# Performance work log

Measured on AMD Instinct MI355X. Metric: run time of the kernel, lower is better.

## Reference

```python
import jax, jax.numpy as jnp
import numpy as np

WS = 7  # window size
NH = 4  # num heads


def _relative_position_index(ws: int) -> np.ndarray:
    coords = np.stack(np.meshgrid(np.arange(ws), np.arange(ws), indexing='ij'))  # [2,ws,ws]
    coords = coords.reshape(2, -1)
    rel = coords[:, :, None] - coords[:, None, :]  # [2,N,N]
    rel = rel.transpose(1, 2, 0) + (ws - 1)
    rel[:, :, 0] *= 2 * ws - 1
    return rel.sum(-1)  # [N,N] in [0,(2ws-1)^2)


REL_IDX = _relative_position_index(WS)


def setup_inputs() -> dict:
    key = jax.random.key(0)
    k1, k2, k3, k4 = jax.random.split(key, 4)
    dim = 128
    x = jax.random.normal(k1, (64, 56, 56, dim), dtype=jnp.float32)
    qkv_w = jax.random.normal(k2, (dim, 3 * dim), dtype=jnp.float32) * (dim ** -0.5)
    qkv_b = jnp.zeros((3 * dim,), dtype=jnp.float32)
    proj_w = jax.random.normal(k3, (dim, dim), dtype=jnp.float32) * (dim ** -0.5)
    proj_b = jnp.zeros((dim,), dtype=jnp.float32)
    bias_table = jax.random.truncated_normal(k4, -2.0, 2.0, ((2 * WS - 1) ** 2, NH), dtype=jnp.float32) * 0.02
    return {"x": x, "qkv_w": qkv_w, "qkv_b": qkv_b, "proj_w": proj_w, "proj_b": proj_b, "bias_table": bias_table}


def reference(x, qkv_w, qkv_b, proj_w, proj_b, bias_table):
    B, H, W, C = x.shape
    ws, nh = WS, NH
    hd = C // nh
    N = ws * ws
    # window partition: [B*nWh*nWw, N, C]  (H,W divisible by ws -> no padding branch)
    xw = x.reshape(B, H // ws, ws, W // ws, ws, C).transpose(0, 1, 3, 2, 4, 5).reshape(-1, N, C)
    qkv = xw @ qkv_w + qkv_b  # [nW, N, 3C]
    qkv = qkv.reshape(-1, N, 3, nh, hd).transpose(2, 0, 3, 1, 4)  # [3, nW, nh, N, hd]
    q, k, v = qkv[0], qkv[1], qkv[2]
    attn = jnp.einsum('whqd,whkd->whqk', q, k) * (hd ** -0.5)  # [nW, nh, N, N]
    rel_bias = bias_table[REL_IDX.reshape(-1)].reshape(N, N, nh).transpose(2, 0, 1)  # [nh,N,N]
    attn = jax.nn.softmax(attn + rel_bias[None], axis=-1)
    out = jnp.einsum('whqk,whkd->whqd', attn, v)  # [nW, nh, N, hd]
    out = out.transpose(0, 2, 1, 3).reshape(-1, N, C)
    out = out @ proj_w + proj_b
    # window reverse
    out = out.reshape(B, H // ws, W // ws, ws, ws, C).transpose(0, 1, 3, 2, 4, 5).reshape(B, H, W, C)
    return out
```

## Files before the change

kernel.cpp:

```cpp
#include <hip/hip_runtime.h>
#include <hip/hip_bf16.h>

#define NTOK 49
#define NPAD 64
#define CDIM 128
#define C3   384
#define NHEAD 4
#define HDIM 32
#define SCALE 0.17677669529663687f

#define QS 136
#define VS 72
#define PS 72

typedef __attribute__((ext_vector_type(8))) __bf16 bf16x8;
typedef __attribute__((ext_vector_type(4))) __bf16 bf16x4;
typedef __attribute__((ext_vector_type(4))) float f32x4;

#define PIN(v) asm volatile("" : "+v"(v))


__global__ __launch_bounds__(256) void prep_kernel(
    const float* __restrict__ qkv_w, const float* __restrict__ proj_w,
    const float* __restrict__ bias_table,
    __bf16* __restrict__ qkvT, __bf16* __restrict__ projT, float* __restrict__ blut)
{
  int o = blockIdx.x * 256 + threadIdx.x;
  if (o < CDIM * C3) {
    int n = o >> 7, k = o & 127;
    float v = qkv_w[k * C3 + n];
    if (n < CDIM) v *= SCALE;
    qkvT[o] = (__bf16)v;
  } else if (o < CDIM * C3 + CDIM * CDIM) {
    int o2 = o - CDIM * C3;
    int n = o2 >> 7, k = o2 & 127;
    projT[o2] = (__bf16)proj_w[k * CDIM + n];
  } else if (o < CDIM * C3 + CDIM * CDIM + NHEAD * NPAD * NPAD) {
    int t3 = o - (CDIM * C3 + CDIM * CDIM);
    int h = t3 >> 12, r = (t3 >> 6) & 63, c = t3 & 63;
    float v;
    if (c >= NTOK) v = -1e30f;
    else if (r >= NTOK) v = 0.0f;
    else {
      int idx = (r / 7 - c / 7 + 6) * 13 + (r % 7 - c % 7 + 6);
      v = bias_table[idx * NHEAD + h];
    }
    blut[t3] = v;
  }
}

__global__ __launch_bounds__(512, 4) void attn_kernel(
    const float* __restrict__ x, const float* __restrict__ qkv_b,
    const float* __restrict__ proj_b,
    const __bf16* __restrict__ qkvT, const __bf16* __restrict__ projT,
    const float* __restrict__ blut, float* __restrict__ out)
{
  __shared__ __align__(16) char smem[71680];
  __bf16* qs_ = (__bf16*)smem;
  __bf16* ks_ = qs_ + NPAD * QS;
  __bf16* vT_ = ks_ + NPAD * QS;
  char*   un_ = (char*)(vT_ + CDIM * VS);
  __bf16* xa_ = (__bf16*)un_;
  __bf16* Pm_ = (__bf16*)un_;

  const int tid  = threadIdx.x;
  const int wave = tid >> 6;
  const int lane = tid & 63;
  const int l15  = lane & 15;
  const int lg   = lane >> 4;

  const int win = blockIdx.x;
  const int b  = win >> 6;
  const int wh = (win >> 3) & 7;
  const int ww = win & 7;
  const float* xbase = x + (((b * 56) + wh * 7) * 56 + ww * 7) * CDIM;

  #pragma unroll
  for (int p = 0; p < 2; ++p) {
    int L = p * 512 + tid;
    int r = L >> 4, c = L & 15;
    bf16x8 v8;
    if (r < NTOK) {
      const float* g = xbase + ((r / 7) * 56 + (r % 7)) * CDIM + c * 8;
      f32x4 x0 = *(const f32x4*)g;
      f32x4 x1 = *(const f32x4*)(g + 4);
      v8[0] = (__bf16)x0[0]; v8[1] = (__bf16)x0[1]; v8[2] = (__bf16)x0[2]; v8[3] = (__bf16)x0[3];
      v8[4] = (__bf16)x1[0]; v8[5] = (__bf16)x1[1]; v8[6] = (__bf16)x1[2]; v8[7] = (__bf16)x1[3];
    } else {
      #pragma unroll
      for (int q2 = 0; q2 < 8; ++q2) v8[q2] = (__bf16)0.0f;
    }
    *(bf16x8*)(xa_ + r * QS + c * 8) = v8;
  }

  const int nb = wave * 48;
  bf16x8 bq[3][4];
  #pragma unroll
  for (int nt = 0; nt < 3; ++nt)
    #pragma unroll
    for (int kt = 0; kt < 4; ++kt) {
      bq[nt][kt] = *(const bf16x8*)(qkvT + (nb + nt * 16 + l15) * CDIM + kt * 32 + lg * 8);
      PIN(bq[nt][kt]);
    }
  float qb[3];
  #pragma unroll
  for (int nt = 0; nt < 3; ++nt) {
    qb[nt] = qkv_b[nb + nt * 16 + l15];
    if (nb + nt * 16 < CDIM) qb[nt] *= SCALE;
  }

  __syncthreads();

  #pragma unroll 2
  for (int mt = 0; mt < 4; ++mt) {
    bf16x8 a[4];
    #pragma unroll
    for (int kt = 0; kt < 4; ++kt)
      a[kt] = *(const bf16x8*)(xa_ + (mt * 16 + l15) * QS + kt * 32 + lg * 8);

    f32x4 acc[3];
    #pragma unroll
    for (int nt = 0; nt < 3; ++nt) { acc[nt][0]=0.f; acc[nt][1]=0.f; acc[nt][2]=0.f; acc[nt][3]=0.f; }
    #pragma unroll
    for (int nt = 0; nt < 3; ++nt)
      #pragma unroll
      for (int kt = 0; kt < 4; ++kt)
        acc[nt] = __builtin_amdgcn_mfma_f32_16x16x32_bf16(a[kt], bq[nt][kt], acc[nt], 0, 0, 0);

    const int r0 = mt * 16 + lg * 4;
    #pragma unroll
    for (int nt = 0; nt < 3; ++nt) {
      const int n = nb + nt * 16 + l15;
      if (n < CDIM) {
        #pragma unroll
        for (int i = 0; i < 4; ++i)
          qs_[(r0 + i) * QS + n] = (__bf16)(acc[nt][i] + qb[nt]);
      } else if (n < 2 * CDIM) {
        #pragma unroll
        for (int i = 0; i < 4; ++i)
          ks_[(r0 + i) * QS + (n - CDIM)] = (__bf16)(acc[nt][i] + qb[nt]);
      } else {
        bf16x4 vv;
        #pragma unroll
        for (int i = 0; i < 4; ++i) vv[i] = (__bf16)(acc[nt][i] + qb[nt]);
        *(bf16x4*)(vT_ + (n - 2 * CDIM) * VS + r0) = vv;
      }
    }
  }
  __syncthreads();

  const int nb2 = wave * 16;
  bf16x8 bp[4];
  #pragma unroll
  for (int kt = 0; kt < 4; ++kt) {
    bp[kt] = *(const bf16x8*)(projT + (nb2 + l15) * CDIM + kt * 32 + lg * 8);
    PIN(bp[kt]);
  }
  const float pb = proj_b[nb2 + l15];

  __bf16* O_ = qs_;

  {
    const int h  = wave & 3;
    const int hc = h * HDIM;
    const float* blh = blut + h * 4096;
    __bf16* Pw = Pm_ + wave * 16 * PS;

    bf16x8 bk[4];
    #pragma unroll
    for (int nt = 0; nt < 4; ++nt)
      bk[nt] = *(const bf16x8*)(ks_ + (nt * 16 + l15) * QS + hc + lg * 8);
    bf16x8 bv[2][2];
    #pragma unroll
    for (int n16 = 0; n16 < 2; ++n16)
      #pragma unroll
      for (int kt = 0; kt < 2; ++kt)
        bv[n16][kt] = *(const bf16x8*)(vT_ + (hc + n16 * 16 + l15) * VS + kt * 32 + lg * 8);

    #pragma unroll
    for (int mi = 0; mi < 2; ++mi) {
      const int mt = (wave >> 2) * 2 + mi;
      const int m0 = mt * 16;

      float bias[4][4];
      #pragma unroll
      for (int i = 0; i < 4; ++i) {
        const int r = m0 + lg * 4 + i;
        #pragma unroll
        for (int c = 0; c < 4; ++c) bias[i][c] = blh[r * 64 + c * 16 + l15];
      }

      bf16x8 aqf = *(const bf16x8*)(qs_ + (m0 + l15) * QS + hc + lg * 8);
      f32x4 s[4];
      #pragma unroll
      for (int nt = 0; nt < 4; ++nt) {
        f32x4 z; z[0]=0.f; z[1]=0.f; z[2]=0.f; z[3]=0.f;
        s[nt] = __builtin_amdgcn_mfma_f32_16x16x32_bf16(aqf, bk[nt], z, 0, 0, 0);
      }
      float inv[4];
      #pragma unroll
      for (int i = 0; i < 4; ++i) {
        const int lr = lg * 4 + i;
        float e0 = __expf(s[0][i] + bias[i][0]);
        float e1 = __expf(s[1][i] + bias[i][1]);
        float e2 = __expf(s[2][i] + bias[i][2]);
        float e3 = __expf(s[3][i] + bias[i][3]);
        Pw[lr * PS +      l15] = (__bf16)e0;
        Pw[lr * PS + 16 + l15] = (__bf16)e1;
        Pw[lr * PS + 32 + l15] = (__bf16)e2;
        Pw[lr * PS + 48 + l15] = (__bf16)e3;
        float sum = (e0 + e1) + (e2 + e3);
        #pragma unroll
        for (int off = 1; off < 16; off <<= 1) sum += __shfl_xor(sum, off);
        inv[i] = __builtin_amdgcn_rcpf(sum);
      }
      f32x4 o0, o1;
      o0[0]=0.f;o0[1]=0.f;o0[2]=0.f;o0[3]=0.f; o1[0]=0.f;o1[1]=0.f;o1[2]=0.f;o1[3]=0.f;
      #pragma unroll
      for (int kt = 0; kt < 2; ++kt) {
        bf16x8 ap = *(const bf16x8*)(Pw + l15 * PS + kt * 32 + lg * 8);
        o0 = __builtin_amdgcn_mfma_f32_16x16x32_bf16(ap, bv[0][kt], o0, 0, 0, 0);
        o1 = __builtin_amdgcn_mfma_f32_16x16x32_bf16(ap, bv[1][kt], o1, 0, 0, 0);
      }
      const int r0 = m0 + lg * 4;
      #pragma unroll
      for (int i = 0; i < 4; ++i) {
        O_[(r0 + i) * QS + hc +      l15] = (__bf16)(o0[i] * inv[i]);
        O_[(r0 + i) * QS + hc + 16 + l15] = (__bf16)(o1[i] * inv[i]);
      }
    }
  }
  __syncthreads();

  float* outw = out + (((b * 56) + wh * 7) * 56 + ww * 7) * CDIM;
  #pragma unroll
  for (int mt = 0; mt < 4; ++mt) {
    bf16x8 ao[4];
    #pragma unroll
    for (int kt = 0; kt < 4; ++kt)
      ao[kt] = *(const bf16x8*)(O_ + (mt * 16 + l15) * QS + kt * 32 + lg * 8);
    f32x4 c0;
    c0[0]=0.f;c0[1]=0.f;c0[2]=0.f;c0[3]=0.f;
    #pragma unroll
    for (int kt = 0; kt < 4; ++kt)
      c0 = __builtin_amdgcn_mfma_f32_16x16x32_bf16(ao[kt], bp[kt], c0, 0, 0, 0);
    #pragma unroll
    for (int i = 0; i < 4; ++i) {
      const int r = mt * 16 + lg * 4 + i;
      if (r < NTOK) {
        float* po = outw + ((r / 7) * 56 + (r % 7)) * CDIM + nb2;
        po[l15] = c0[i] + pb;
      }
    }
  }
}

extern "C" void kernel_launch(void* const* d_in, const int* in_sizes, int n_in,
                              void* d_out, int out_size, void* d_ws, size_t ws_size,
                              hipStream_t stream) {
  const float* x          = (const float*)d_in[0];
  const float* qkv_w      = (const float*)d_in[1];
  const float* qkv_b      = (const float*)d_in[2];
  const float* proj_w     = (const float*)d_in[3];
  const float* proj_b     = (const float*)d_in[4];
  const float* bias_table = (const float*)d_in[5];

  __bf16* qkvT  = (__bf16*)d_ws;
  __bf16* projT = qkvT + C3 * CDIM;
  float*  blut  = (float*)((char*)d_ws + 131072);
  float*  out   = (float*)d_out;

  hipLaunchKernelGGL(prep_kernel, dim3(320), dim3(256), 0, stream,
                     qkv_w, proj_w, bias_table, qkvT, projT, blut);
  hipLaunchKernelGGL(attn_kernel, dim3(4096), dim3(512), 0, stream,
                     x, qkv_b, proj_b, qkvT, projT, blut, out);
}
```

Before: 267.0 us.

## Reorder QKV projection to alias shared buffers and raise occupancy

Splits the QKV projection so K and V are computed and stored first, while Q stays in registers until the x tile is no longer needed. This lets x share memory with Q and P share memory with V, cutting LDS per block so the launch bound can target 6 blocks per CU instead of 4. The score MFMA is transposed (K as the A operand), which makes the bias loads vectorised and the softmax row sums a two-step cross-lane reduction instead of a four-step one. It also makes the prep kernel's weight reads coalesced and its writes strided. In exchange it adds an extra barrier, keeps Q accumulators live across it (more register pressure), and the tighter launch bound risks spills.

```diff
diff --git a/kernel.cpp b/kernel.cpp
--- a/kernel.cpp
+++ b/kernel.cpp
@@ -27,41 +27,41 @@
 {
   int o = blockIdx.x * 256 + threadIdx.x;
   if (o < CDIM * C3) {
-    int n = o >> 7, k = o & 127;
-    float v = qkv_w[k * C3 + n];
+    int k = o / C3, n = o - k * C3;
+    float v = qkv_w[o];
     if (n < CDIM) v *= SCALE;
-    qkvT[o] = (__bf16)v;
+    qkvT[n * CDIM + k] = (__bf16)v;
   } else if (o < CDIM * C3 + CDIM * CDIM) {
     int o2 = o - CDIM * C3;
-    int n = o2 >> 7, k = o2 & 127;
-    projT[o2] = (__bf16)proj_w[k * CDIM + n];
+    int k = o2 >> 7, n = o2 & 127;
+    projT[n * CDIM + k] = (__bf16)proj_w[o2];
   } else if (o < CDIM * C3 + CDIM * CDIM + NHEAD * NPAD * NPAD) {
     int t3 = o - (CDIM * C3 + CDIM * CDIM);
-    int h = t3 >> 12, r = (t3 >> 6) & 63, c = t3 & 63;
+    int hh = t3 >> 12, r = (t3 >> 6) & 63, c = t3 & 63;
     float v;
     if (c >= NTOK) v = -1e30f;
     else if (r >= NTOK) v = 0.0f;
     else {
       int idx = (r / 7 - c / 7 + 6) * 13 + (r % 7 - c % 7 + 6);
-      v = bias_table[idx * NHEAD + h];
+      v = bias_table[idx * NHEAD + hh];
     }
     blut[t3] = v;
   }
 }
 
-__global__ __launch_bounds__(512, 4) void attn_kernel(
+__global__ __launch_bounds__(512, 6) void attn_kernel(
     const float* __restrict__ x, const float* __restrict__ qkv_b,
     const float* __restrict__ proj_b,
     const __bf16* __restrict__ qkvT, const __bf16* __restrict__ projT,
     const float* __restrict__ blut, float* __restrict__ out)
 {
-  __shared__ __align__(16) char smem[71680];
+  __shared__ __align__(16) char smem[53248];
   __bf16* qs_ = (__bf16*)smem;
   __bf16* ks_ = qs_ + NPAD * QS;
   __bf16* vT_ = ks_ + NPAD * QS;
-  char*   un_ = (char*)(vT_ + CDIM * VS);
-  __bf16* xa_ = (__bf16*)un_;
-  __bf16* Pm_ = (__bf16*)un_;
+  __bf16* xa_ = qs_;
+  __bf16* Pm_ = vT_;
+  __bf16* O_  = qs_;
 
   const int tid  = threadIdx.x;
   const int wave = tid >> 6;
@@ -93,61 +93,144 @@
     *(bf16x8*)(xa_ + r * QS + c * 8) = v8;
   }
 
-  const int nb = wave * 48;
-  bf16x8 bq[3][4];
-  #pragma unroll
-  for (int nt = 0; nt < 3; ++nt)
+  const int nch = wave * 16 + l15;
+  bf16x8 bwk[4], bwv[4];
+  #pragma unroll
+  for (int kt = 0; kt < 4; ++kt) {
+    bwk[kt] = *(const bf16x8*)(qkvT + (CDIM + nch) * CDIM + kt * 32 + lg * 8);     PIN(bwk[kt]);
+    bwv[kt] = *(const bf16x8*)(qkvT + (2 * CDIM + nch) * CDIM + kt * 32 + lg * 8); PIN(bwv[kt]);
+  }
+  const float kb = qkv_b[CDIM + nch];
+  const float vb = qkv_b[2 * CDIM + nch];
+
+  __syncthreads();
+
+  #pragma unroll 2
+  for (int mt = 0; mt < 4; ++mt) {
+    bf16x8 a[4];
+    #pragma unroll
+    for (int kt = 0; kt < 4; ++kt)
+      a[kt] = *(const bf16x8*)(xa_ + (mt * 16 + l15) * QS + kt * 32 + lg * 8);
+    f32x4 ck, cv;
+    ck[0]=0.f; ck[1]=0.f; ck[2]=0.f; ck[3]=0.f;
+    cv[0]=0.f; cv[1]=0.f; cv[2]=0.f; cv[3]=0.f;
     #pragma unroll
     for (int kt = 0; kt < 4; ++kt) {
-      bq[nt][kt] = *(const bf16x8*)(qkvT + (nb + nt * 16 + l15) * CDIM + kt * 32 + lg * 8);
-      PIN(bq[nt][kt]);
-    }
-  float qb[3];
-  #pragma unroll
-  for (int nt = 0; nt < 3; ++nt) {
-    qb[nt] = qkv_b[nb + nt * 16 + l15];
-    if (nb + nt * 16 < CDIM) qb[nt] *= SCALE;
-  }
-
-  __syncthreads();
-
-  #pragma unroll 2
+      ck = __builtin_amdgcn_mfma_f32_16x16x32_bf16(a[kt], bwk[kt], ck, 0, 0, 0);
+      cv = __builtin_amdgcn_mfma_f32_16x16x32_bf16(a[kt], bwv[kt], cv, 0, 0, 0);
+    }
+    const int r0 = mt * 16 + lg * 4;
+    #pragma unroll
+    for (int i = 0; i < 4; ++i)
+      ks_[(r0 + i) * QS + nch] = (__bf16)(ck[i] + kb);
+    bf16x4 vv;
+    #pragma unroll
+    for (int i = 0; i < 4; ++i) vv[i] = (__bf16)(cv[i] + vb);
+    *(bf16x4*)(vT_ + nch * VS + r0) = vv;
+  }
+
+  bf16x8 bwq[4];
+  #pragma unroll
+  for (int kt = 0; kt < 4; ++kt) {
+    bwq[kt] = *(const bf16x8*)(qkvT + nch * CDIM + kt * 32 + lg * 8); PIN(bwq[kt]);
+  }
+  const float qb = qkv_b[nch] * SCALE;
+  f32x4 aq[4];
+  #pragma unroll
   for (int mt = 0; mt < 4; ++mt) {
     bf16x8 a[4];
     #pragma unroll
     for (int kt = 0; kt < 4; ++kt)
       a[kt] = *(const bf16x8*)(xa_ + (mt * 16 + l15) * QS + kt * 32 + lg * 8);
-
-    f32x4 acc[3];
-    #pragma unroll
-    for (int nt = 0; nt < 3; ++nt) { acc[nt][0]=0.f; acc[nt][1]=0.f; acc[nt][2]=0.f; acc[nt][3]=0.f; }
-    #pragma unroll
-    for (int nt = 0; nt < 3; ++nt)
+    aq[mt][0]=0.f; aq[mt][1]=0.f; aq[mt][2]=0.f; aq[mt][3]=0.f;
+    #pragma unroll
+    for (int kt = 0; kt < 4; ++kt)
+      aq[mt] = __builtin_amdgcn_mfma_f32_16x16x32_bf16(a[kt], bwq[kt], aq[mt], 0, 0, 0);
+  }
+
+  __syncthreads();
+
+  const int h  = wave & 3;
+  const int hc = h * HDIM;
+  bf16x8 akf[4];
+  #pragma unroll
+  for (int nt = 0; nt < 4; ++nt)
+    akf[nt] = *(const bf16x8*)(ks_ + (nt * 16 + l15) * QS + hc + lg * 8);
+  bf16x8 bv[2][2];
+  #pragma unroll
+  for (int n16 = 0; n16 < 2; ++n16)
+    #pragma unroll
+    for (int kt = 0; kt < 2; ++kt)
+      bv[n16][kt] = *(const bf16x8*)(vT_ + (hc + n16 * 16 + l15) * VS + kt * 32 + lg * 8);
+
+  #pragma unroll
+  for (int mt = 0; mt < 4; ++mt) {
+    const int r0 = mt * 16 + lg * 4;
+    #pragma unroll
+    for (int i = 0; i < 4; ++i)
+      qs_[(r0 + i) * QS + nch] = (__bf16)(aq[mt][i] + qb);
+  }
+
+  __syncthreads();
+
+  const float* blh = blut + h * 4096;
+  __bf16* Pw = Pm_ + wave * 16 * PS;
+
+  #pragma unroll
+  for (int mi = 0; mi < 2; ++mi) {
+    const int m0 = ((wave >> 2) * 2 + mi) * 16;
+
+    f32x4 bias[4];
+    #pragma unroll
+    for (int nt = 0; nt < 4; ++nt)
+      bias[nt] = *(const f32x4*)(blh + (m0 + l15) * 64 + nt * 16 + lg * 4);
+
+    bf16x8 qf = *(const bf16x8*)(qs_ + (m0 + l15) * QS + hc + lg * 8);
+    f32x4 s[4];
+    #pragma unroll
+    for (int nt = 0; nt < 4; ++nt) {
+      f32x4 z; z[0]=0.f; z[1]=0.f; z[2]=0.f; z[3]=0.f;
+      s[nt] = __builtin_amdgcn_mfma_f32_16x16x32_bf16(akf[nt], qf, z, 0, 0, 0);
+    }
+
+    float es[4][4];
+    float p0 = 0.f, p1 = 0.f;
+    #pragma unroll
+    for (int nt = 0; nt < 4; ++nt) {
       #pragma unroll
-      for (int kt = 0; kt < 4; ++kt)
-        acc[nt] = __builtin_amdgcn_mfma_f32_16x16x32_bf16(a[kt], bq[nt][kt], acc[nt], 0, 0, 0);
-
-    const int r0 = mt * 16 + lg * 4;
-    #pragma unroll
-    for (int nt = 0; nt < 3; ++nt) {
-      const int n = nb + nt * 16 + l15;
-      if (n < CDIM) {
-        #pragma unroll
-        for (int i = 0; i < 4; ++i)
-          qs_[(r0 + i) * QS + n] = (__bf16)(acc[nt][i] + qb[nt]);
-      } else if (n < 2 * CDIM) {
-        #pragma unroll
-        for (int i = 0; i < 4; ++i)
-          ks_[(r0 + i) * QS + (n - CDIM)] = (__bf16)(acc[nt][i] + qb[nt]);
-      } else {
-        bf16x4 vv;
-        #pragma unroll
-        for (int i = 0; i < 4; ++i) vv[i] = (__bf16)(acc[nt][i] + qb[nt]);
-        *(bf16x4*)(vT_ + (n - 2 * CDIM) * VS + r0) = vv;
+      for (int i = 0; i < 4; ++i) {
+        float e = __expf(s[nt][i] + bias[nt][i]);
+        es[nt][i] = e;
+        if (nt & 1) p1 += e; else p0 += e;
       }
-    }
-  }
-  __syncthreads();
+      bf16x4 pv;
+      #pragma unroll
+      for (int i = 0; i < 4; ++i) pv[i] = (__bf16)es[nt][i];
+      *(bf16x4*)(Pw + l15 * PS + nt * 16 + lg * 4) = pv;
+    }
+    float psum = p0 + p1;
+    psum += __shfl_xor(psum, 16);
+    psum += __shfl_xor(psum, 32);
+    const float inv = __builtin_amdgcn_rcpf(psum);
+
+    f32x4 o0, o1;
+    o0[0]=0.f;o0[1]=0.f;o0[2]=0.f;o0[3]=0.f; o1[0]=0.f;o1[1]=0.f;o1[2]=0.f;o1[3]=0.f;
+    #pragma unroll
+    for (int kt = 0; kt < 2; ++kt) {
+      bf16x8 ap = *(const bf16x8*)(Pw + l15 * PS + kt * 32 + lg * 8);
+      o0 = __builtin_amdgcn_mfma_f32_16x16x32_bf16(ap, bv[0][kt], o0, 0, 0, 0);
+      o1 = __builtin_amdgcn_mfma_f32_16x16x32_bf16(ap, bv[1][kt], o1, 0, 0, 0);
+    }
+    float invr[4];
+    #pragma unroll
+    for (int i = 0; i < 4; ++i) invr[i] = __shfl(inv, lg * 4 + i);
+    const int r0 = m0 + lg * 4;
+    #pragma unroll
+    for (int i = 0; i < 4; ++i) {
+      O_[(r0 + i) * QS + hc +      l15] = (__bf16)(o0[i] * invr[i]);
+      O_[(r0 + i) * QS + hc + 16 + l15] = (__bf16)(o1[i] * invr[i]);
+    }
+  }
 
   const int nb2 = wave * 16;
   bf16x8 bp[4];
@@ -158,78 +241,6 @@
   }
   const float pb = proj_b[nb2 + l15];
 
-  __bf16* O_ = qs_;
-
-  {
-    const int h  = wave & 3;
-    const int hc = h * HDIM;
-    const float* blh = blut + h * 4096;
-    __bf16* Pw = Pm_ + wave * 16 * PS;
-
-    bf16x8 bk[4];
-    #pragma unroll
-    for (int nt = 0; nt < 4; ++nt)
-      bk[nt] = *(const bf16x8*)(ks_ + (nt * 16 + l15) * QS + hc + lg * 8);
-    bf16x8 bv[2][2];
-    #pragma unroll
-    for (int n16 = 0; n16 < 2; ++n16)
-      #pragma unroll
-      for (int kt = 0; kt < 2; ++kt)
-        bv[n16][kt] = *(const bf16x8*)(vT_ + (hc + n16 * 16 + l15) * VS + kt * 32 + lg * 8);
-
-    #pragma unroll
-    for (int mi = 0; mi < 2; ++mi) {
-      const int mt = (wave >> 2) * 2 + mi;
-      const int m0 = mt * 16;
-
-      float bias[4][4];
-      #pragma unroll
-      for (int i = 0; i < 4; ++i) {
-        const int r = m0 + lg * 4 + i;
-        #pragma unroll
-        for (int c = 0; c < 4; ++c) bias[i][c] = blh[r * 64 + c * 16 + l15];
-      }
-
-      bf16x8 aqf = *(const bf16x8*)(qs_ + (m0 + l15) * QS + hc + lg * 8);
-      f32x4 s[4];
-      #pragma unroll
-      for (int nt = 0; nt < 4; ++nt) {
-        f32x4 z; z[0]=0.f; z[1]=0.f; z[2]=0.f; z[3]=0.f;
-        s[nt] = __builtin_amdgcn_mfma_f32_16x16x32_bf16(aqf, bk[nt], z, 0, 0, 0);
-      }
-      float inv[4];
-      #pragma unroll
-      for (int i = 0; i < 4; ++i) {
-        const int lr = lg * 4 + i;
-        float e0 = __expf(s[0][i] + bias[i][0]);
-        float e1 = __expf(s[1][i] + bias[i][1]);
-        float e2 = __expf(s[2][i] + bias[i][2]);
-        float e3 = __expf(s[3][i] + bias[i][3]);
-        Pw[lr * PS +      l15] = (__bf16)e0;
-        Pw[lr * PS + 16 + l15] = (__bf16)e1;
-        Pw[lr * PS + 32 + l15] = (__bf16)e2;
-        Pw[lr * PS + 48 + l15] = (__bf16)e3;
-        float sum = (e0 + e1) + (e2 + e3);
-        #pragma unroll
-        for (int off = 1; off < 16; off <<= 1) sum += __shfl_xor(sum, off);
-        inv[i] = __builtin_amdgcn_rcpf(sum);
-      }
-      f32x4 o0, o1;
-      o0[0]=0.f;o0[1]=0.f;o0[2]=0.f;o0[3]=0.f; o1[0]=0.f;o1[1]=0.f;o1[2]=0.f;o1[3]=0.f;
-      #pragma unroll
-      for (int kt = 0; kt < 2; ++kt) {
-        bf16x8 ap = *(const bf16x8*)(Pw + l15 * PS + kt * 32 + lg * 8);
-        o0 = __builtin_amdgcn_mfma_f32_16x16x32_bf16(ap, bv[0][kt], o0, 0, 0, 0);
-        o1 = __builtin_amdgcn_mfma_f32_16x16x32_bf16(ap, bv[1][kt], o1, 0, 0, 0);
-      }
-      const int r0 = m0 + lg * 4;
-      #pragma unroll
-      for (int i = 0; i < 4; ++i) {
-        O_[(r0 + i) * QS + hc +      l15] = (__bf16)(o0[i] * inv[i]);
-        O_[(r0 + i) * QS + hc + 16 + l15] = (__bf16)(o1[i] * inv[i]);
-      }
-    }
-  }
   __syncthreads();
 
   float* outw = out + (((b * 56) + wh * 7) * 56 + ww * 7) * CDIM;
```

Measured after the change: 262.1 us. No clear change (-1.9%).
